# Kernel tuning notes

Measured on AMD Instinct MI355X. Metric: run time of the kernel, lower is better.

Reference implementation:

```python
import jax, jax.numpy as jnp
import numpy as np

N = 50000      # nodes
E = 800000     # edges (before self loops)
F = 128        # node_feat_dim
HID = 128      # hidden_dim
LN_EPS = 1e-5
NEG_SLOPE = 0.2


def setup_inputs() -> dict:
    key = jax.random.key(0)
    ks = jax.random.split(key, 32)
    g = lambda k, shape, s=0.05: jax.random.normal(k, shape, dtype=jnp.float32) * s
    inp = {}
    inp["x"] = jax.random.normal(ks[0], (N, F), dtype=jnp.float32)
    inp["edge_index"] = jax.random.randint(ks[1], (2, E), 0, N)
    i = 2
    # conv1: F -> 4 heads x 32, concat -> HID
    inp["W1l"] = g(ks[i], (F, HID)); inp["b1l"] = jnp.zeros((HID,), jnp.float32)
    inp["W1r"] = g(ks[i+1], (F, HID)); inp["b1r"] = jnp.zeros((HID,), jnp.float32)
    inp["a1"] = g(ks[i+2], (4, HID // 4)); inp["c1"] = jnp.zeros((HID,), jnp.float32)
    inp["g1"] = jnp.ones((HID,), jnp.float32); inp["be1"] = jnp.zeros((HID,), jnp.float32)
    # conv2: HID -> 4 heads x 32, concat -> HID
    inp["W2l"] = g(ks[i+3], (HID, HID)); inp["b2l"] = jnp.zeros((HID,), jnp.float32)
    inp["W2r"] = g(ks[i+4], (HID, HID)); inp["b2r"] = jnp.zeros((HID,), jnp.float32)
    inp["a2"] = g(ks[i+5], (4, HID // 4)); inp["c2"] = jnp.zeros((HID,), jnp.float32)
    inp["g2"] = jnp.ones((HID,), jnp.float32); inp["be2"] = jnp.zeros((HID,), jnp.float32)
    # conv3: HID -> 1 head x HID, mean -> HID
    inp["W3l"] = g(ks[i+6], (HID, HID)); inp["b3l"] = jnp.zeros((HID,), jnp.float32)
    inp["W3r"] = g(ks[i+7], (HID, HID)); inp["b3r"] = jnp.zeros((HID,), jnp.float32)
    inp["a3"] = g(ks[i+8], (1, HID)); inp["c3"] = jnp.zeros((HID,), jnp.float32)
    inp["g3"] = jnp.ones((HID,), jnp.float32); inp["be3"] = jnp.zeros((HID,), jnp.float32)
    return inp


def _gatv2(x, Wl, bl, Wr, br, att, bias, src, dst, heads, outc, concat):
    """GATv2Conv: xl=source transform, xr=target transform, edge-wise
    LeakyReLU attention, per-destination segment softmax, scatter-add."""
    n = x.shape[0]
    xl = (x @ Wl + bl).reshape(n, heads, outc)   # lin_l -> source (x_j)
    e_feat = jax.nn.leaky_relu(xl[src] + ((x @ Wr + br).reshape(n, heads, outc))[dst], NEG_SLOPE)  # [E,H,C]
    logits = jnp.einsum('ehc,hc->eh', e_feat, att)                 # [E,H]
    m = jax.ops.segment_max(logits, dst, num_segments=n)           # [N,H]
    a = jnp.exp(logits - m[dst])
    denom = jax.ops.segment_sum(a, dst, num_segments=n)            # [N,H]
    a = a / denom[dst]
    out = jax.ops.segment_sum(xl[src] * a[:, :, None], dst, num_segments=n)  # [N,H,C]
    out = out.reshape(n, heads * outc) if concat else out.mean(axis=1)
    return out + bias


def _ln(h, g, b):
    mu = h.mean(-1, keepdims=True)
    var = ((h - mu) ** 2).mean(-1, keepdims=True)
    return (h - mu) * jax.lax.rsqrt(var + LN_EPS) * g + b


def reference(x, edge_index,
              W1l, b1l, W1r, b1r, a1, c1, g1, be1,
              W2l, b2l, W2r, b2r, a2, c2, g2, be2,
              W3l, b3l, W3r, b3r, a3, c3, g3, be3):
    n = x.shape[0]
    loops = jnp.arange(n, dtype=edge_index.dtype)
    src = jnp.concatenate([edge_index[0], loops])  # add_self_loops=True
    dst = jnp.concatenate([edge_index[1], loops])
    h = _gatv2(x, W1l, b1l, W1r, b1r, a1, c1, src, dst, 4, HID // 4, True)
    h = jax.nn.relu(_ln(h, g1, be1))  # dropout is identity in eval
    h = _gatv2(h, W2l, b2l, W2r, b2r, a2, c2, src, dst, 4, HID // 4, True)
    h = jax.nn.relu(_ln(h, g2, be2))
    h = _gatv2(h, W3l, b3l, W3r, b3r, a3, c3, src, dst, 1, HID, False)
    h = jax.nn.relu(_ln(h, g3, be3))
    return h
```

## Files before the change

### kernel.cpp

```cpp
#include <hip/hip_runtime.h>


typedef __attribute__((ext_vector_type(8))) short bf16x8;
typedef __attribute__((ext_vector_type(4))) float f32x4;

__device__ __forceinline__ ushort f2bf(float f) {
    unsigned u = __float_as_uint(f);
    unsigned r = (u + 0x7fffu + ((u >> 16) & 1u)) >> 16;
    return (ushort)r;
}
__device__ __forceinline__ float bflo(unsigned u) { return __uint_as_float(u << 16); }
__device__ __forceinline__ float bfhi(unsigned u) { return __uint_as_float(u & 0xffff0000u); }


__global__ __launch_bounds__(256) void cvt_kernel(const float* __restrict__ src,
                                                  ushort* __restrict__ dst, int n4) {
    int i = blockIdx.x * 256 + threadIdx.x;
    if (i >= n4) return;
    float4 v = ((const float4*)src)[i];
    ushort4 o;
    o.x = f2bf(v.x); o.y = f2bf(v.y); o.z = f2bf(v.z); o.w = f2bf(v.w);
    ((ushort4*)dst)[i] = o;
}

__global__ __launch_bounds__(256) void wT_kernel(const float* W0, const float* W1,
                                                 const float* W2, const float* W3,
                                                 const float* W4, const float* W5,
                                                 ushort* __restrict__ WT) {
    __shared__ ushort s[128 * 129];
    const float* Ws[6] = {W0, W1, W2, W3, W4, W5};
    const float* W = Ws[blockIdx.x];
    ushort* O = WT + blockIdx.x * 16384;
    int tid = threadIdx.x;
    for (int r = 0; r < 128; r += 2) {
        int k = r + (tid >> 7);
        int nn = tid & 127;
        s[nn * 129 + k] = f2bf(W[k * 128 + nn]);
    }
    __syncthreads();
    for (int i = tid; i < 16384; i += 256) {
        int nn = i >> 7, k = i & 127;
        O[i] = s[nn * 129 + k];
    }
}


__global__ void histogram_kernel(const int* __restrict__ dstrow, int E, int n,
                                 int* __restrict__ counts) {
    int i = blockIdx.x * 256 + threadIdx.x;
    int ET = E + n;
    if (i >= ET) return;
    int d = (i < E) ? dstrow[i] : (i - E);
    atomicAdd(&counts[d], 1);
}

__global__ __launch_bounds__(256) void block_reduce_kernel(const int* __restrict__ counts,
                                                           int n, int* __restrict__ partials) {
    int b = blockIdx.x, tid = threadIdx.x;
    int base = b * 1024 + tid * 4;
    int c0 = 0, c1 = 0, c2 = 0, c3 = 0;
    if (base + 3 < n) {
        int4 v = *(const int4*)&counts[base];
        c0 = v.x; c1 = v.y; c2 = v.z; c3 = v.w;
    } else {
        if (base < n) c0 = counts[base];
        if (base + 1 < n) c1 = counts[base + 1];
        if (base + 2 < n) c2 = counts[base + 2];
        if (base + 3 < n) c3 = counts[base + 3];
    }
    int t = c0 + c1 + c2 + c3;
    #pragma unroll
    for (int d = 1; d < 64; d <<= 1) t += __shfl_xor(t, d, 64);
    __shared__ int ws[4];
    if ((tid & 63) == 0) ws[tid >> 6] = t;
    __syncthreads();
    if (tid == 0) partials[b] = ws[0] + ws[1] + ws[2] + ws[3];
}

__global__ void scan_partials_kernel(int* __restrict__ partials, int nb,
                                     int* __restrict__ rowptr, int n) {
    int lane = threadIdx.x;
    int v = (lane < nb) ? partials[lane] : 0;
    int x = v;
    #pragma unroll
    for (int d = 1; d < 64; d <<= 1) {
        int t = __shfl_up(x, d, 64);
        if (lane >= d) x += t;
    }
    if (lane < nb) partials[lane] = x - v;
    if (lane == 63) rowptr[n] = x;
}

__global__ __launch_bounds__(256) void block_scan_kernel(int* __restrict__ counts_cursor,
                                                         const int* __restrict__ partials,
                                                         int n, int* __restrict__ rowptr) {
    int b = blockIdx.x, tid = threadIdx.x;
    int lane = tid & 63, wv = tid >> 6;
    int base = b * 1024 + tid * 4;
    int c0 = 0, c1 = 0, c2 = 0, c3 = 0;
    if (base + 3 < n) {
        int4 v = *(const int4*)&counts_cursor[base];
        c0 = v.x; c1 = v.y; c2 = v.z; c3 = v.w;
    } else {
        if (base < n) c0 = counts_cursor[base];
        if (base + 1 < n) c1 = counts_cursor[base + 1];
        if (base + 2 < n) c2 = counts_cursor[base + 2];
        if (base + 3 < n) c3 = counts_cursor[base + 3];
    }
    int t = c0 + c1 + c2 + c3;
    int x = t;
    #pragma unroll
    for (int d = 1; d < 64; d <<= 1) {
        int tt = __shfl_up(x, d, 64);
        if (lane >= d) x += tt;
    }
    __shared__ int ws[4];
    if (lane == 63) ws[wv] = x;
    __syncthreads();
    int woff = 0;
    for (int j = 0; j < 4; ++j) woff += (j < wv) ? ws[j] : 0;
    int excl = x - t + woff + partials[b];
    if (base < n)     { rowptr[base] = excl;               counts_cursor[base] = excl; }
    if (base + 1 < n) { rowptr[base + 1] = excl + c0;      counts_cursor[base + 1] = excl + c0; }
    if (base + 2 < n) { rowptr[base + 2] = excl + c0 + c1; counts_cursor[base + 2] = excl + c0 + c1; }
    if (base + 3 < n) { rowptr[base + 3] = excl + c0 + c1 + c2; counts_cursor[base + 3] = excl + c0 + c1 + c2; }
}

__global__ void scatter_kernel(const int* __restrict__ srcrow, const int* __restrict__ dstrow,
                               int E, int n, int* __restrict__ cursor, int* __restrict__ srcs) {
    int i = blockIdx.x * 256 + threadIdx.x;
    int ET = E + n;
    if (i >= ET) return;
    int s, d;
    if (i < E) { s = srcrow[i]; d = dstrow[i]; } else { s = i - E; d = s; }
    int pos = atomicAdd(&cursor[d], 1);
    srcs[pos] = s << 8;
}


__global__ __launch_bounds__(256) void dual_gemm_mfma(
    const ushort* __restrict__ A,
    const ushort* __restrict__ WTl, const ushort* __restrict__ WTr,
    const float* __restrict__ bl, const float* __restrict__ br,
    ushort* __restrict__ XL, ushort* __restrict__ XR, int n) {
    int tid = threadIdx.x;
    int wid = tid >> 6, lane = tid & 63;
    int ln15 = lane & 15, hi = lane >> 4;
    int row0 = blockIdx.x * 64;

    const ushort* WT  = (wid < 2) ? WTl : WTr;
    const float* bias = (wid < 2) ? bl : br;
    ushort* OUT       = (wid < 2) ? XL : XR;
    int colbase = (wid & 1) * 64;

    float bv[4];
    #pragma unroll
    for (int nn = 0; nn < 4; ++nn) bv[nn] = bias[colbase + nn * 16 + ln15];

    f32x4 acc[4][4];
    #pragma unroll
    for (int m = 0; m < 4; ++m)
        #pragma unroll
        for (int nn = 0; nn < 4; ++nn) acc[m][nn] = (f32x4){0.f, 0.f, 0.f, 0.f};

    #pragma unroll
    for (int kk = 0; kk < 4; ++kk) {
        int kb = kk * 64 + hi * 16;
        bf16x8 a[4], b[4];
        #pragma unroll
        for (int m = 0; m < 4; ++m) {
            int r = row0 + m * 16 + ln15;
            a[m] = *(const bf16x8*)((const char*)A + (size_t)r * 256 + kb);
        }
        #pragma unroll
        for (int nn = 0; nn < 4; ++nn) {
            int c = colbase + nn * 16 + ln15;
            b[nn] = *(const bf16x8*)((const char*)WT + (size_t)c * 256 + kb);
        }
        #pragma unroll
        for (int m = 0; m < 4; ++m)
            #pragma unroll
            for (int nn = 0; nn < 4; ++nn)
                acc[m][nn] = __builtin_amdgcn_mfma_f32_16x16x32_bf16(a[m], b[nn], acc[m][nn], 0, 0, 0);
    }

    #pragma unroll
    for (int m = 0; m < 4; ++m)
        #pragma unroll
        for (int r = 0; r < 4; ++r) {
            int row = row0 + m * 16 + hi * 4 + r;
            if (row < n) {
                #pragma unroll
                for (int nn = 0; nn < 4; ++nn) {
                    int c = colbase + nn * 16 + ln15;
                    OUT[(size_t)row * 128 + c] = f2bf(acc[m][nn][r] + bv[nn]);
                }
            }
        }
}


#define UNPACK8(u, a)                                            \
    { a[0] = bflo(u.x); a[1] = bfhi(u.x); a[2] = bflo(u.y);      \
      a[3] = bfhi(u.y); a[4] = bflo(u.z); a[5] = bfhi(u.z);      \
      a[6] = bflo(u.w); a[7] = bfhi(u.w); }

template <int H, bool OUT_BF16>
__global__ __launch_bounds__(256) void aggregate_kernel(
    const ushort* __restrict__ XL, const ushort* __restrict__ XR,
    const int* __restrict__ rowptr, const int* __restrict__ srcs,
    const float* __restrict__ att, const float* __restrict__ bias,
    const float* __restrict__ gamma, const float* __restrict__ beta,
    void* __restrict__ OUTP, int n) {
    int tid = threadIdx.x;
    int wid = tid >> 6, lane = tid & 63;
    int g = lane >> 4, l = lane & 15;
    int node = blockIdx.x * 16 + wid * 4 + g;
    bool alive = (node < n);
    int c0 = l * 8;
    constexpr int GS = (128 / H) / 8;

    const char* XLc = (const char*)XL;
    int lb = l * 16;

    float at[8];
    {
        float4 a0 = *(const float4*)&att[c0];
        float4 a1 = *(const float4*)&att[c0 + 4];
        at[0] = a0.x; at[1] = a0.y; at[2] = a0.z; at[3] = a0.w;
        at[4] = a1.x; at[5] = a1.y; at[6] = a1.z; at[7] = a1.w;
        #pragma unroll
        for (int j = 0; j < 8; ++j) at[j] *= 1.44269504f;
    }

    float xr[8];
    int s = 0, e = 0;
    if (alive) {
        uint4 ur = *(const uint4*)(XLc + 0 + ((size_t)node << 8) + lb + ((size_t)((const char*)XR - XLc)));
        UNPACK8(ur, xr);
        s = rowptr[node]; e = rowptr[node + 1];
    } else {
        #pragma unroll
        for (int j = 0; j < 8; ++j) xr[j] = 0.f;
    }

    float acc[8];
    #pragma unroll
    for (int j = 0; j < 8; ++j) acc[j] = 0.f;
    float den = 0.f;

    int i = s;
    for (; i + 2 <= e; i += 2) {
        int o0 = srcs[i], o1 = srcs[i + 1];
        uint4 u0 = *(const uint4*)(XLc + o0 + lb);
        uint4 u1 = *(const uint4*)(XLc + o1 + lb);
        float a[8], b[8];
        UNPACK8(u0, a);
        UNPACK8(u1, b);
        float p = 0.f, p2 = 0.f, q = 0.f, q2 = 0.f;
        #pragma unroll
        for (int j = 0; j < 8; j += 2) {
            float t0 = a[j] + xr[j], t1 = a[j + 1] + xr[j + 1];
            t0 = fmaxf(t0, 0.2f * t0); t1 = fmaxf(t1, 0.2f * t1);
            p = fmaf(t0, at[j], p); p2 = fmaf(t1, at[j + 1], p2);
            float s0 = b[j] + xr[j], s1 = b[j + 1] + xr[j + 1];
            s0 = fmaxf(s0, 0.2f * s0); s1 = fmaxf(s1, 0.2f * s1);
            q = fmaf(s0, at[j], q); q2 = fmaf(s1, at[j + 1], q2);
        }
        p += p2; q += q2;
        #pragma unroll
        for (int d = 1; d < GS; d <<= 1) {
            p += __shfl_xor(p, d, 64);
            q += __shfl_xor(q, d, 64);
        }
        float ew = exp2f(p), eq = exp2f(q);
        #pragma unroll
        for (int j = 0; j < 8; ++j) acc[j] = fmaf(ew, a[j], fmaf(eq, b[j], acc[j]));
        den += ew + eq;
    }
    if (i < e) {
        int o0 = srcs[i];
        uint4 u0 = *(const uint4*)(XLc + o0 + lb);
        float a[8];
        UNPACK8(u0, a);
        float p = 0.f, p2 = 0.f;
        #pragma unroll
        for (int j = 0; j < 8; j += 2) {
            float t0 = a[j] + xr[j], t1 = a[j + 1] + xr[j + 1];
            t0 = fmaxf(t0, 0.2f * t0); t1 = fmaxf(t1, 0.2f * t1);
            p = fmaf(t0, at[j], p); p2 = fmaf(t1, at[j + 1], p2);
        }
        p += p2;
        #pragma unroll
        for (int d = 1; d < GS; d <<= 1) p += __shfl_xor(p, d, 64);
        float ew = exp2f(p);
        #pragma unroll
        for (int j = 0; j < 8; ++j) acc[j] = fmaf(ew, a[j], acc[j]);
        den += ew;
    }

    float inv = 1.f / den;
    float o[8];
    {
        float4 b0 = *(const float4*)&bias[c0];
        float4 b1 = *(const float4*)&bias[c0 + 4];
        o[0] = fmaf(acc[0], inv, b0.x); o[1] = fmaf(acc[1], inv, b0.y);
        o[2] = fmaf(acc[2], inv, b0.z); o[3] = fmaf(acc[3], inv, b0.w);
        o[4] = fmaf(acc[4], inv, b1.x); o[5] = fmaf(acc[5], inv, b1.y);
        o[6] = fmaf(acc[6], inv, b1.z); o[7] = fmaf(acc[7], inv, b1.w);
    }

    float ssum = 0.f;
    #pragma unroll
    for (int j = 0; j < 8; ++j) ssum += o[j];
    #pragma unroll
    for (int d = 1; d < 16; d <<= 1) ssum += __shfl_xor(ssum, d, 64);
    float mu = ssum * (1.f / 128.f);
    float vsum = 0.f;
    #pragma unroll
    for (int j = 0; j < 8; ++j) { float dd = o[j] - mu; vsum += dd * dd; }
    #pragma unroll
    for (int d = 1; d < 16; d <<= 1) vsum += __shfl_xor(vsum, d, 64);
    float rstd = rsqrtf(vsum * (1.f / 128.f) + 1e-5f);

    if (!alive) return;

    float4 g0 = *(const float4*)&gamma[c0];
    float4 g1 = *(const float4*)&gamma[c0 + 4];
    float4 e0 = *(const float4*)&beta[c0];
    float4 e1 = *(const float4*)&beta[c0 + 4];
    float gm[8] = {g0.x, g0.y, g0.z, g0.w, g1.x, g1.y, g1.z, g1.w};
    float bt[8] = {e0.x, e0.y, e0.z, e0.w, e1.x, e1.y, e1.z, e1.w};
    float y[8];
    #pragma unroll
    for (int j = 0; j < 8; ++j)
        y[j] = fmaxf(fmaf((o[j] - mu) * rstd, gm[j], bt[j]), 0.f);

    if (OUT_BF16) {
        uint4 ov;
        ov.x = ((unsigned)f2bf(y[1]) << 16) | f2bf(y[0]);
        ov.y = ((unsigned)f2bf(y[3]) << 16) | f2bf(y[2]);
        ov.z = ((unsigned)f2bf(y[5]) << 16) | f2bf(y[4]);
        ov.w = ((unsigned)f2bf(y[7]) << 16) | f2bf(y[6]);
        *(uint4*)&((ushort*)OUTP)[(size_t)node * 128 + c0] = ov;
    } else {
        float* O = (float*)OUTP + (size_t)node * 128 + c0;
        *(float4*)O = make_float4(y[0], y[1], y[2], y[3]);
        *(float4*)(O + 4) = make_float4(y[4], y[5], y[6], y[7]);
    }
}


extern "C" void kernel_launch(void* const* d_in, const int* in_sizes, int n_in,
                              void* d_out, int out_size, void* d_ws, size_t ws_size,
                              hipStream_t stream) {
    const float* x  = (const float*)d_in[0];
    const int*   ei = (const int*)d_in[1];
    const float *W1l = (const float*)d_in[2],  *b1l = (const float*)d_in[3];
    const float *W1r = (const float*)d_in[4],  *b1r = (const float*)d_in[5];
    const float *a1  = (const float*)d_in[6],  *c1  = (const float*)d_in[7];
    const float *g1  = (const float*)d_in[8],  *be1 = (const float*)d_in[9];
    const float *W2l = (const float*)d_in[10], *b2l = (const float*)d_in[11];
    const float *W2r = (const float*)d_in[12], *b2r = (const float*)d_in[13];
    const float *a2  = (const float*)d_in[14], *c2  = (const float*)d_in[15];
    const float *g2  = (const float*)d_in[16], *be2 = (const float*)d_in[17];
    const float *W3l = (const float*)d_in[18], *b3l = (const float*)d_in[19];
    const float *W3r = (const float*)d_in[20], *b3r = (const float*)d_in[21];
    const float *a3  = (const float*)d_in[22], *c3  = (const float*)d_in[23];
    const float *g3  = (const float*)d_in[24], *be3 = (const float*)d_in[25];

    int n  = in_sizes[0] / 128;
    int E  = in_sizes[1] / 2;
    int ET = E + n;
    size_t nPad = (size_t)((n + 63) / 64) * 64;

    char* ws = (char*)d_ws;
    ushort* xb = (ushort*)ws;                      ws += nPad * 128 * 2;
    ushort* XL = (ushort*)ws;                      ws += nPad * 128 * 2;
    ushort* XR = (ushort*)ws;                      ws += nPad * 128 * 2;
    ushort* hb = (ushort*)ws;                      ws += nPad * 128 * 2;
    ushort* WT = (ushort*)ws;                      ws += 6 * 16384 * 2;
    int* rowptr   = (int*)ws;                      ws += (n + 1) * 4;
    int* cursor   = (int*)ws;                      ws += n * 4;
    int* partials = (int*)ws;                      ws += 64 * 4;
    int* srcs     = (int*)ws;

    const int* srcrow = ei;
    const int* dstrow = ei + E;

    cvt_kernel<<<(n * 128 / 4 + 255) / 256, 256, 0, stream>>>(x, xb, n * 128 / 4);
    wT_kernel<<<6, 256, 0, stream>>>(W1l, W1r, W2l, W2r, W3l, W3r, WT);

    hipMemsetAsync(cursor, 0, (size_t)n * sizeof(int), stream);
    int eb = (ET + 255) / 256;
    int nb = (n + 1023) / 1024;
    histogram_kernel<<<eb, 256, 0, stream>>>(dstrow, E, n, cursor);
    block_reduce_kernel<<<nb, 256, 0, stream>>>(cursor, n, partials);
    scan_partials_kernel<<<1, 64, 0, stream>>>(partials, nb, rowptr, n);
    block_scan_kernel<<<nb, 256, 0, stream>>>(cursor, partials, n, rowptr);
    scatter_kernel<<<eb, 256, 0, stream>>>(srcrow, dstrow, E, n, cursor, srcs);

    int gb = (int)(nPad / 64);
    int ab = (n + 15) / 16;

    dual_gemm_mfma<<<gb, 256, 0, stream>>>(xb, WT + 0 * 16384, WT + 1 * 16384, b1l, b1r, XL, XR, n);
    aggregate_kernel<4, true><<<ab, 256, 0, stream>>>(XL, XR, rowptr, srcs, a1, c1, g1, be1, hb, n);
    dual_gemm_mfma<<<gb, 256, 0, stream>>>(hb, WT + 2 * 16384, WT + 3 * 16384, b2l, b2r, XL, XR, n);
    aggregate_kernel<4, true><<<ab, 256, 0, stream>>>(XL, XR, rowptr, srcs, a2, c2, g2, be2, hb, n);
    dual_gemm_mfma<<<gb, 256, 0, stream>>>(hb, WT + 4 * 16384, WT + 5 * 16384, b3l, b3r, XL, XR, n);
    aggregate_kernel<1, false><<<ab, 256, 0, stream>>>(XL, XR, rowptr, srcs, a3, c3, g3, be3, d_out, n);
}
```

Baseline: 431.4 us.

## Partition CSR build atomics by destination range per XCD

Replaces the one-thread-per-edge histogram and scatter kernels with versions where each block handles one of eight destination-node ranges, picked by blockIdx modulo 8. Every edge chunk is scanned by eight blocks, and each block only performs atomics for destinations in its own range. The intent is for atomics on a given counter to come from a single XCD and stay local to its L2, reducing cross-die atomic traffic. In exchange, the edge index array is read eight times and each block runs a grid-stride loop. The XR address computation in the aggregate kernel is also simplified.

```diff
diff --git a/kernel.cpp b/kernel.cpp
--- a/kernel.cpp
+++ b/kernel.cpp
@@ -3,6 +3,8 @@
 
 typedef __attribute__((ext_vector_type(8))) short bf16x8;
 typedef __attribute__((ext_vector_type(4))) float f32x4;
+
+#define NPART 8
 
 __device__ __forceinline__ ushort f2bf(float f) {
     unsigned u = __float_as_uint(f);
@@ -45,14 +47,45 @@
 }
 
 
-__global__ void histogram_kernel(const int* __restrict__ dstrow, int E, int n,
-                                 int* __restrict__ counts) {
-    int i = blockIdx.x * 256 + threadIdx.x;
+__global__ __launch_bounds__(256) void histogram_part_kernel(
+    const int* __restrict__ dstrow, int E, int n, int* __restrict__ counts) {
+    int part = blockIdx.x & 7;
+    int sub = blockIdx.x >> 3;
+    int nsub = gridDim.x >> 3;
+    int ppn = (n + NPART - 1) / NPART;
+    int lo = part * ppn;
+    int hi = lo + ppn; if (hi > n) hi = n;
     int ET = E + n;
-    if (i >= ET) return;
-    int d = (i < E) ? dstrow[i] : (i - E);
-    atomicAdd(&counts[d], 1);
-}
+    int chunk = (ET + nsub - 1) / nsub;
+    int s0 = sub * chunk, s1 = s0 + chunk; if (s1 > ET) s1 = ET;
+    for (int i = s0 + threadIdx.x; i < s1; i += 256) {
+        int d = (i < E) ? dstrow[i] : (i - E);
+        if (d >= lo && d < hi) atomicAdd(&counts[d], 1);
+    }
+}
+
+__global__ __launch_bounds__(256) void scatter_part_kernel(
+    const int* __restrict__ srcrow, const int* __restrict__ dstrow,
+    int E, int n, int* __restrict__ cursor, int* __restrict__ srcs) {
+    int part = blockIdx.x & 7;
+    int sub = blockIdx.x >> 3;
+    int nsub = gridDim.x >> 3;
+    int ppn = (n + NPART - 1) / NPART;
+    int lo = part * ppn;
+    int hi = lo + ppn; if (hi > n) hi = n;
+    int ET = E + n;
+    int chunk = (ET + nsub - 1) / nsub;
+    int s0 = sub * chunk, s1 = s0 + chunk; if (s1 > ET) s1 = ET;
+    for (int i = s0 + threadIdx.x; i < s1; i += 256) {
+        int d = (i < E) ? dstrow[i] : (i - E);
+        if (d >= lo && d < hi) {
+            int s = (i < E) ? srcrow[i] : (i - E);
+            int pos = atomicAdd(&cursor[d], 1);
+            srcs[pos] = s << 8;
+        }
+    }
+}
+
 
 __global__ __launch_bounds__(256) void block_reduce_kernel(const int* __restrict__ counts,
                                                            int n, int* __restrict__ partials) {
@@ -126,17 +159,6 @@
     if (base + 3 < n) { rowptr[base + 3] = excl + c0 + c1 + c2; counts_cursor[base + 3] = excl + c0 + c1 + c2; }
 }
 
-__global__ void scatter_kernel(const int* __restrict__ srcrow, const int* __restrict__ dstrow,
-                               int E, int n, int* __restrict__ cursor, int* __restrict__ srcs) {
-    int i = blockIdx.x * 256 + threadIdx.x;
-    int ET = E + n;
-    if (i >= ET) return;
-    int s, d;
-    if (i < E) { s = srcrow[i]; d = dstrow[i]; } else { s = i - E; d = s; }
-    int pos = atomicAdd(&cursor[d], 1);
-    srcs[pos] = s << 8;
-}
-
 
 __global__ __launch_bounds__(256) void dual_gemm_mfma(
     const ushort* __restrict__ A,
@@ -236,7 +258,7 @@
     float xr[8];
     int s = 0, e = 0;
     if (alive) {
-        uint4 ur = *(const uint4*)(XLc + 0 + ((size_t)node << 8) + lb + ((size_t)((const char*)XR - XLc)));
+        uint4 ur = *(const uint4*)((const char*)XR + ((size_t)node << 8) + lb);
         UNPACK8(ur, xr);
         s = rowptr[node]; e = rowptr[node + 1];
     } else {
@@ -371,7 +393,6 @@
 
     int n  = in_sizes[0] / 128;
     int E  = in_sizes[1] / 2;
-    int ET = E + n;
     size_t nPad = (size_t)((n + 63) / 64) * 64;
 
     char* ws = (char*)d_ws;
@@ -392,13 +413,12 @@
     wT_kernel<<<6, 256, 0, stream>>>(W1l, W1r, W2l, W2r, W3l, W3r, WT);
 
     hipMemsetAsync(cursor, 0, (size_t)n * sizeof(int), stream);
-    int eb = (ET + 255) / 256;
     int nb = (n + 1023) / 1024;
-    histogram_kernel<<<eb, 256, 0, stream>>>(dstrow, E, n, cursor);
+    histogram_part_kernel<<<2048, 256, 0, stream>>>(dstrow, E, n, cursor);
     block_reduce_kernel<<<nb, 256, 0, stream>>>(cursor, n, partials);
     scan_partials_kernel<<<1, 64, 0, stream>>>(partials, nb, rowptr, n);
     block_scan_kernel<<<nb, 256, 0, stream>>>(cursor, partials, n, rowptr);
-    scatter_kernel<<<eb, 256, 0, stream>>>(srcrow, dstrow, E, n, cursor, srcs);
+    scatter_part_kernel<<<2048, 256, 0, stream>>>(srcrow, dstrow, E, n, cursor, srcs);
 
     int gb = (int)(nPad / 64);
     int ab = (n + 15) / 16;
```

New measurement: 417.2 us. 3.3% less time.
